# Performance work log

Measured on AMD Instinct MI355X. Metric: run time of the kernel, lower is better.

Reference implementation:

```python
import jax, jax.numpy as jnp
import numpy as np

INPUT_SIZE = 1024
NUM_QUBITS = 12
EMBED_SIZE = 2 ** NUM_QUBITS  # 4096
BATCH = 4096


def setup_inputs() -> dict:
    key = jax.random.key(0)
    k_x, k_w, k_p = jax.random.split(key, 3)
    x = jax.random.normal(k_x, (BATCH, INPUT_SIZE), dtype=jnp.float32)
    quantum_weights = jax.random.normal(k_w, (INPUT_SIZE, EMBED_SIZE), dtype=jnp.float32)
    quantum_phases = jax.random.normal(k_p, (INPUT_SIZE, NUM_QUBITS), dtype=jnp.float32)
    return {"x": x, "quantum_weights": quantum_weights, "quantum_phases": quantum_phases}


def reference(x, quantum_weights, quantum_phases):
    # Original: out[b] = Re( sum_j exp(i * mean(phases[j]) * x[b,j]) * W[j,:] ).
    # W is real, so the real part is sum_j cos(mean(phases[j]) * x[b,j]) * W[j,:],
    # i.e. a cosine-modulated matmul.
    phase_mean = jnp.mean(quantum_phases, axis=1)          # [input_size]
    coef = jnp.cos(x * phase_mean[None, :])                # [batch, input_size]
    return coef @ quantum_weights                          # [batch, embed_size]
```

## Files before the change

kernel.cpp:

```cpp
#include <hip/hip_runtime.h>
#include <hip/hip_bf16.h>


#define K_DIM 1024
#define N_DIM 4096
#define B_DIM 4096
#define NQ 12

typedef __attribute__((ext_vector_type(8))) _Float16 f16x8;
typedef __attribute__((ext_vector_type(4))) float f32x4;


__global__ void pm_kernel(const float* __restrict__ phases, float* __restrict__ pm) {
    int j = blockIdx.x * 256 + threadIdx.x;
    if (j < K_DIM) {
        float s = 0.f;
#pragma unroll
        for (int q = 0; q < NQ; ++q) s += phases[j * NQ + q];
        pm[j] = s * (1.0f / NQ);
    }
}

__global__ void asplit_kernel(const float* __restrict__ x, const float* __restrict__ pm,
                              char* __restrict__ Ah, char* __restrict__ Al) {
    int i = blockIdx.x * 256 + threadIdx.x;
    int row = i >> 7;
    int k0  = (i & 127) << 3;
    const float* xp = x + ((size_t)row << 10) + k0;
    float4 xa = *(const float4*)xp;
    float4 xb = *(const float4*)(xp + 4);
    float4 pa = *(const float4*)(pm + k0);
    float4 pb = *(const float4*)(pm + k0 + 4);
    float c[8];
    c[0] = __cosf(xa.x * pa.x); c[1] = __cosf(xa.y * pa.y);
    c[2] = __cosf(xa.z * pa.z); c[3] = __cosf(xa.w * pa.w);
    c[4] = __cosf(xb.x * pb.x); c[5] = __cosf(xb.y * pb.y);
    c[6] = __cosf(xb.z * pb.z); c[7] = __cosf(xb.w * pb.w);
    f16x8 hv, lv;
#pragma unroll
    for (int j = 0; j < 8; ++j) {
        _Float16 h = (_Float16)c[j];
        hv[j] = h;
        lv[j] = (_Float16)(c[j] - (float)h);
    }
    int tm = row >> 7, kt = k0 >> 6;
    int r = row & 127, kk = k0 & 63;
    size_t base = ((size_t)tm * 16 + (size_t)kt) * 16384;
    int addr = ((r << 7) + (kk << 1)) ^ ((r & 7) << 4);
    *(f16x8*)(Ah + base + addr) = hv;
    *(f16x8*)(Al + base + addr) = lv;
}

__global__ void wsplit_kernel(const float* __restrict__ W, char* __restrict__ Bf) {
    __shared__ float t[64][65];
    int n0 = blockIdx.x * 64, k0 = blockIdx.y * 64;
    int tid = threadIdx.x;
#pragma unroll
    for (int p = 0; p < 16; ++p) {
        int lin = p * 256 + tid;
        int kk = lin >> 6, nn = lin & 63;
        t[kk][nn] = W[(size_t)(k0 + kk) * N_DIM + n0 + nn];
    }
    __syncthreads();
    size_t base = ((size_t)(n0 >> 7) * 16 + (size_t)blockIdx.y) * 16384;
#pragma unroll
    for (int p2 = 0; p2 < 2; ++p2) {
        int w = p2 * 256 + tid;
        int nn = w >> 3, oct = w & 7;
        int r = (n0 & 127) + nn;
        f16x8 hv;
#pragma unroll
        for (int j = 0; j < 8; ++j) hv[j] = (_Float16)t[oct * 8 + j][nn];
        int addr = ((r << 7) + (oct << 4)) ^ ((r & 7) << 4);
        *(f16x8*)(Bf + base + addr) = hv;
    }
}

#define GLL16(g, l)                                                           \
    __builtin_amdgcn_global_load_lds(                                         \
        (const __attribute__((address_space(1))) void*)(g),                   \
        (__attribute__((address_space(3))) void*)(l), 16, 0, 0)

__global__ __launch_bounds__(256, 2) void gemm_kernel(
        const char* __restrict__ Ah, const char* __restrict__ Al,
        const char* __restrict__ Bf, float* __restrict__ C) {
    __shared__ char lds[49152];
    const int tid  = threadIdx.x;
    const int lane = tid & 63;
    const int wid  = tid >> 6;
    const int wr = wid >> 1, wc = wid & 1;
    const int fr   = lane & 15;
    const int colb = (lane >> 4) << 4;

    const char* pAh = Ah + (size_t)blockIdx.y * 16 * 16384;
    const char* pAl = Al + (size_t)blockIdx.y * 16 * 16384;
    const char* pBf = Bf + (size_t)blockIdx.x * 16 * 16384;

    int aAddr[4][2], bAddr[4][2];
#pragma unroll
    for (int m = 0; m < 4; ++m) {
        int r = wr * 64 + m * 16 + fr;
#pragma unroll
        for (int kh = 0; kh < 2; ++kh)
            aAddr[m][kh] = ((r << 7) + kh * 64 + colb) ^ ((r & 7) << 4);
    }
#pragma unroll
    for (int n = 0; n < 4; ++n) {
        int r = wc * 64 + n * 16 + fr;
#pragma unroll
        for (int kh = 0; kh < 2; ++kh)
            bAddr[n][kh] = ((r << 7) + kh * 64 + colb) ^ ((r & 7) << 4);
    }

    f32x4 acc[4][4];
#pragma unroll
    for (int m = 0; m < 4; ++m)
#pragma unroll
        for (int n = 0; n < 4; ++n)
            acc[m][n] = (f32x4){0.f, 0.f, 0.f, 0.f};

    for (int kt = 0; kt < K_DIM / 64; ++kt) {
#pragma unroll
        for (int p = 0; p < 4; ++p) {
            int off = p * 4096 + (tid << 4);
            GLL16(pAh + off, lds + off);
            GLL16(pAl + off, lds + 16384 + off);
            GLL16(pBf + off, lds + 32768 + off);
        }
        pAh += 16384; pAl += 16384; pBf += 16384;
        __syncthreads();

#pragma unroll
        for (int kh = 0; kh < 2; ++kh) {
            f16x8 aH[4], aL[4], bF[4];
#pragma unroll
            for (int m = 0; m < 4; ++m) {
                aH[m] = *(const f16x8*)(lds + aAddr[m][kh]);
                aL[m] = *(const f16x8*)(lds + 16384 + aAddr[m][kh]);
            }
#pragma unroll
            for (int n = 0; n < 4; ++n)
                bF[n] = *(const f16x8*)(lds + 32768 + bAddr[n][kh]);
#pragma unroll
            for (int m = 0; m < 4; ++m)
#pragma unroll
                for (int n = 0; n < 4; ++n) {
                    acc[m][n] = __builtin_amdgcn_mfma_f32_16x16x32_f16(aH[m], bF[n], acc[m][n], 0, 0, 0);
                    acc[m][n] = __builtin_amdgcn_mfma_f32_16x16x32_f16(aL[m], bF[n], acc[m][n], 0, 0, 0);
                }
        }
        __syncthreads();
    }

    const int crow0 = blockIdx.y * 128 + wr * 64 + ((lane >> 4) << 2);
    const int ccol0 = blockIdx.x * 128 + wc * 64 + fr;
#pragma unroll
    for (int m = 0; m < 4; ++m)
#pragma unroll
        for (int n = 0; n < 4; ++n) {
            size_t base = (size_t)(crow0 + m * 16) * N_DIM + (size_t)(ccol0 + n * 16);
#pragma unroll
            for (int j = 0; j < 4; ++j)
                C[base + (size_t)j * N_DIM] = acc[m][n][j];
        }
}

extern "C" void kernel_launch(void* const* d_in, const int* in_sizes, int n_in,
                              void* d_out, int out_size, void* d_ws, size_t ws_size,
                              hipStream_t stream) {
    const float* x      = (const float*)d_in[0];
    const float* W      = (const float*)d_in[1];
    const float* phases = (const float*)d_in[2];
    float* out = (float*)d_out;

    char* ws = (char*)d_ws;
    float* pm = (float*)ws;
    char* Ah = ws + 65536;
    char* Al = Ah + (size_t)8 * 1024 * 1024;
    char* Bf = Al + (size_t)8 * 1024 * 1024;

    pm_kernel<<<4, 256, 0, stream>>>(phases, pm);
    asplit_kernel<<<(B_DIM * (K_DIM / 8)) / 256, 256, 0, stream>>>(x, pm, Ah, Al);
    wsplit_kernel<<<dim3(N_DIM / 64, K_DIM / 64), 256, 0, stream>>>(W, Bf);
    gemm_kernel<<<dim3(N_DIM / 128, B_DIM / 128), 256, 0, stream>>>(Ah, Al, Bf, out);
}
```

Baseline: 152.4 us.

## Drop fp16 low-part split and use 256x256 triple-buffered MFMA GEMM

```diff
diff --git a/kernel.cpp b/kernel.cpp
--- a/kernel.cpp
+++ b/kernel.cpp
@@ -22,7 +22,7 @@
 }
 
 __global__ void asplit_kernel(const float* __restrict__ x, const float* __restrict__ pm,
-                              char* __restrict__ Ah, char* __restrict__ Al) {
+                              char* __restrict__ Ah) {
     int i = blockIdx.x * 256 + threadIdx.x;
     int row = i >> 7;
     int k0  = (i & 127) << 3;
@@ -31,24 +31,16 @@
     float4 xb = *(const float4*)(xp + 4);
     float4 pa = *(const float4*)(pm + k0);
     float4 pb = *(const float4*)(pm + k0 + 4);
-    float c[8];
-    c[0] = __cosf(xa.x * pa.x); c[1] = __cosf(xa.y * pa.y);
-    c[2] = __cosf(xa.z * pa.z); c[3] = __cosf(xa.w * pa.w);
-    c[4] = __cosf(xb.x * pb.x); c[5] = __cosf(xb.y * pb.y);
-    c[6] = __cosf(xb.z * pb.z); c[7] = __cosf(xb.w * pb.w);
-    f16x8 hv, lv;
-#pragma unroll
-    for (int j = 0; j < 8; ++j) {
-        _Float16 h = (_Float16)c[j];
-        hv[j] = h;
-        lv[j] = (_Float16)(c[j] - (float)h);
-    }
-    int tm = row >> 7, kt = k0 >> 6;
-    int r = row & 127, kk = k0 & 63;
-    size_t base = ((size_t)tm * 16 + (size_t)kt) * 16384;
-    int addr = ((r << 7) + (kk << 1)) ^ ((r & 7) << 4);
+    f16x8 hv;
+    hv[0] = (_Float16)__cosf(xa.x * pa.x); hv[1] = (_Float16)__cosf(xa.y * pa.y);
+    hv[2] = (_Float16)__cosf(xa.z * pa.z); hv[3] = (_Float16)__cosf(xa.w * pa.w);
+    hv[4] = (_Float16)__cosf(xb.x * pb.x); hv[5] = (_Float16)__cosf(xb.y * pb.y);
+    hv[6] = (_Float16)__cosf(xb.z * pb.z); hv[7] = (_Float16)__cosf(xb.w * pb.w);
+    int tm = row >> 8, kt = k0 >> 5;
+    int r = row & 255, kk = k0 & 31;
+    size_t base = ((size_t)tm * 32 + (size_t)kt) * 16384;
+    int addr = ((r << 6) + (kk << 1)) ^ ((r & 7) << 4);
     *(f16x8*)(Ah + base + addr) = hv;
-    *(f16x8*)(Al + base + addr) = lv;
 }
 
 __global__ void wsplit_kernel(const float* __restrict__ W, char* __restrict__ Bf) {
@@ -62,16 +54,19 @@
         t[kk][nn] = W[(size_t)(k0 + kk) * N_DIM + n0 + nn];
     }
     __syncthreads();
-    size_t base = ((size_t)(n0 >> 7) * 16 + (size_t)blockIdx.y) * 16384;
+    int tn = n0 >> 8;
 #pragma unroll
     for (int p2 = 0; p2 < 2; ++p2) {
         int w = p2 * 256 + tid;
         int nn = w >> 3, oct = w & 7;
-        int r = (n0 & 127) + nn;
+        int r = (n0 & 255) + nn;
+        int kt = (k0 >> 5) + (oct >> 2);
+        int kk = (oct & 3) * 8;
         f16x8 hv;
 #pragma unroll
         for (int j = 0; j < 8; ++j) hv[j] = (_Float16)t[oct * 8 + j][nn];
-        int addr = ((r << 7) + (oct << 4)) ^ ((r & 7) << 4);
+        size_t base = ((size_t)tn * 32 + (size_t)kt) * 16384;
+        int addr = ((r << 6) + (kk << 1)) ^ ((r & 7) << 4);
         *(f16x8*)(Bf + base + addr) = hv;
     }
 }
@@ -81,81 +76,91 @@
         (const __attribute__((address_space(1))) void*)(g),                   \
         (__attribute__((address_space(3))) void*)(l), 16, 0, 0)
 
-__global__ __launch_bounds__(256, 2) void gemm_kernel(
-        const char* __restrict__ Ah, const char* __restrict__ Al,
-        const char* __restrict__ Bf, float* __restrict__ C) {
-    __shared__ char lds[49152];
+__global__ __launch_bounds__(512, 2) void gemm_kernel(
+        const char* __restrict__ Ah, const char* __restrict__ Bf,
+        float* __restrict__ C) {
+    __shared__ char lds[98304];
     const int tid  = threadIdx.x;
     const int lane = tid & 63;
     const int wid  = tid >> 6;
-    const int wr = wid >> 1, wc = wid & 1;
+    const int wm = wid >> 2, wn = wid & 3;
     const int fr   = lane & 15;
     const int colb = (lane >> 4) << 4;
 
-    const char* pAh = Ah + (size_t)blockIdx.y * 16 * 16384;
-    const char* pAl = Al + (size_t)blockIdx.y * 16 * 16384;
-    const char* pBf = Bf + (size_t)blockIdx.x * 16 * 16384;
+    int wg  = blockIdx.x;
+    int swz = (wg & 7) * 32 + (wg >> 3);
+    int by = swz >> 4, bx = swz & 15;
 
-    int aAddr[4][2], bAddr[4][2];
+    const char* pA = Ah + (size_t)by * 32 * 16384;
+    const char* pB = Bf + (size_t)bx * 32 * 16384;
+
+    int aAddr[8], bAddr[4];
 #pragma unroll
-    for (int m = 0; m < 4; ++m) {
-        int r = wr * 64 + m * 16 + fr;
-#pragma unroll
-        for (int kh = 0; kh < 2; ++kh)
-            aAddr[m][kh] = ((r << 7) + kh * 64 + colb) ^ ((r & 7) << 4);
+    for (int m = 0; m < 8; ++m) {
+        int r = wm * 128 + m * 16 + fr;
+        aAddr[m] = ((r << 6) + colb) ^ ((r & 7) << 4);
     }
 #pragma unroll
     for (int n = 0; n < 4; ++n) {
-        int r = wc * 64 + n * 16 + fr;
-#pragma unroll
-        for (int kh = 0; kh < 2; ++kh)
-            bAddr[n][kh] = ((r << 7) + kh * 64 + colb) ^ ((r & 7) << 4);
+        int r = wn * 64 + n * 16 + fr;
+        bAddr[n] = ((r << 6) + colb) ^ ((r & 7) << 4);
     }
 
-    f32x4 acc[4][4];
+    const int so = tid << 4;
+
 #pragma unroll
-    for (int m = 0; m < 4; ++m)
+    for (int t = 0; t < 2; ++t) {
+        char* d = lds + t * 32768;
+        const char* sA = pA + t * 16384;
+        const char* sB = pB + t * 16384;
+        GLL16(sA + so, d + so);
+        GLL16(sA + 8192 + so, d + 8192 + so);
+        GLL16(sB + so, d + 16384 + so);
+        GLL16(sB + 8192 + so, d + 24576 + so);
+    }
+
+    f32x4 acc[8][4];
+#pragma unroll
+    for (int m = 0; m < 8; ++m)
 #pragma unroll
         for (int n = 0; n < 4; ++n)
             acc[m][n] = (f32x4){0.f, 0.f, 0.f, 0.f};
 
-    for (int kt = 0; kt < K_DIM / 64; ++kt) {
+    for (int t = 0; t < 32; ++t) {
+        asm volatile("s_waitcnt vmcnt(4)" ::: "memory");
+        __builtin_amdgcn_s_barrier();
+        __builtin_amdgcn_sched_barrier(0);
+
+        int t2 = (t + 2) & 31;
+        char* d2 = lds + ((t + 2) % 3) * 32768;
+        const char* sA = pA + t2 * 16384;
+        const char* sB = pB + t2 * 16384;
+        GLL16(sA + so, d2 + so);
+        GLL16(sA + 8192 + so, d2 + 8192 + so);
+        GLL16(sB + so, d2 + 16384 + so);
+        GLL16(sB + 8192 + so, d2 + 24576 + so);
+
+        const char* bufA = lds + (t % 3) * 32768;
+        const char* bufB = bufA + 16384;
+        f16x8 aH[8], bF[4];
 #pragma unroll
-        for (int p = 0; p < 4; ++p) {
-            int off = p * 4096 + (tid << 4);
-            GLL16(pAh + off, lds + off);
-            GLL16(pAl + off, lds + 16384 + off);
-            GLL16(pBf + off, lds + 32768 + off);
-        }
-        pAh += 16384; pAl += 16384; pBf += 16384;
-        __syncthreads();
+        for (int m = 0; m < 8; ++m) aH[m] = *(const f16x8*)(bufA + aAddr[m]);
+#pragma unroll
+        for (int n = 0; n < 4; ++n) bF[n] = *(const f16x8*)(bufB + bAddr[n]);
 
+        __builtin_amdgcn_s_setprio(1);
 #pragma unroll
-        for (int kh = 0; kh < 2; ++kh) {
-            f16x8 aH[4], aL[4], bF[4];
-#pragma unroll
-            for (int m = 0; m < 4; ++m) {
-                aH[m] = *(const f16x8*)(lds + aAddr[m][kh]);
-                aL[m] = *(const f16x8*)(lds + 16384 + aAddr[m][kh]);
-            }
+        for (int m = 0; m < 8; ++m)
 #pragma unroll
             for (int n = 0; n < 4; ++n)
-                bF[n] = *(const f16x8*)(lds + 32768 + bAddr[n][kh]);
-#pragma unroll
-            for (int m = 0; m < 4; ++m)
-#pragma unroll
-                for (int n = 0; n < 4; ++n) {
-                    acc[m][n] = __builtin_amdgcn_mfma_f32_16x16x32_f16(aH[m], bF[n], acc[m][n], 0, 0, 0);
-                    acc[m][n] = __builtin_amdgcn_mfma_f32_16x16x32_f16(aL[m], bF[n], acc[m][n], 0, 0, 0);
-                }
-        }
-        __syncthreads();
+                acc[m][n] = __builtin_amdgcn_mfma_f32_16x16x32_f16(aH[m], bF[n], acc[m][n], 0, 0, 0);
+        __builtin_amdgcn_s_setprio(0);
     }
 
-    const int crow0 = blockIdx.y * 128 + wr * 64 + ((lane >> 4) << 2);
-    const int ccol0 = blockIdx.x * 128 + wc * 64 + fr;
+    const int crow0 = by * 256 + wm * 128 + ((lane >> 4) << 2);
+    const int ccol0 = bx * 256 + wn * 64 + fr;
 #pragma unroll
-    for (int m = 0; m < 4; ++m)
+    for (int m = 0; m < 8; ++m)
 #pragma unroll
         for (int n = 0; n < 4; ++n) {
             size_t base = (size_t)(crow0 + m * 16) * N_DIM + (size_t)(ccol0 + n * 16);
@@ -176,11 +181,10 @@
     char* ws = (char*)d_ws;
     float* pm = (float*)ws;
     char* Ah = ws + 65536;
-    char* Al = Ah + (size_t)8 * 1024 * 1024;
-    char* Bf = Al + (size_t)8 * 1024 * 1024;
+    char* Bf = Ah + (size_t)8 * 1024 * 1024;
 
     pm_kernel<<<4, 256, 0, stream>>>(phases, pm);
-    asplit_kernel<<<(B_DIM * (K_DIM / 8)) / 256, 256, 0, stream>>>(x, pm, Ah, Al);
+    asplit_kernel<<<(B_DIM * (K_DIM / 8)) / 256, 256, 0, stream>>>(x, pm, Ah);
     wsplit_kernel<<<dim3(N_DIM / 64, K_DIM / 64), 256, 0, stream>>>(W, Bf);
-    gemm_kernel<<<dim3(N_DIM / 128, B_DIM / 128), 256, 0, stream>>>(Ah, Al, Bf, out);
+    gemm_kernel<<<256, 512, 0, stream>>>(Ah, Bf, out);
 }
```

Measured after the change: 135.1 us. 1.13x faster.
